# Kernel optimization log

Hardware: AMD Instinct MI355X
Metric: run time of the kernel (lower is better)

The kernel has to match this reference:

```python
import jax, jax.numpy as jnp
import numpy as np

KH, KW = 3, 3
KN = KH * KW  # kernel_n = 9


def _grid_offset(H, W):
    # Faithful to TF build(): stack(meshgrid(ij)).reshape(-1, 2) -- note this
    # interleaves i- and j- grids in an unusual layout; we replicate it exactly.
    init = jnp.stack(jnp.meshgrid(jnp.arange(KH), jnp.arange(KW), indexing='ij'))
    init = init.reshape(-1, 2).astype(jnp.float32)  # (KN, 2)
    ph, pw = (KH - 1) // 2, (KW - 1) // 2
    g = jnp.stack(
        jnp.meshgrid(jnp.arange(-ph, H - ph), jnp.arange(-pw, W - pw), indexing='ij'),
        axis=-1,
    ).astype(jnp.float32)  # (H, W, 2)
    return g[:, :, None, :] + init[None, None]  # (H, W, KN, 2)


def _bilinear_sample(x, coords):
    # x: (B, H, W, C); coords: (B, H, W, KN, 2) with (row, col) float coords.
    B = x.shape[0]
    y, xc = coords[..., 0], coords[..., 1]
    y0 = jnp.floor(y).astype(jnp.int32)
    y1 = jnp.ceil(y).astype(jnp.int32)   # ceil (not floor+1), faithful to TF code
    x0 = jnp.floor(xc).astype(jnp.int32)
    x1 = jnp.ceil(xc).astype(jnp.int32)
    bidx = jnp.arange(B)[:, None, None, None]

    def g(yy, xx):
        return x[bidx, yy, xx]  # (B, H, W, KN, C)

    v_lt = g(y0, x0)
    v_rb = g(y1, x1)
    v_lb = g(y0, x1)  # (lt_row, rb_col) per TF coords_lb
    v_rt = g(y1, x0)  # (rb_row, lt_col) per TF coords_rt
    fy = (y - y0.astype(y.dtype))[..., None]
    fx = (xc - x0.astype(xc.dtype))[..., None]
    v_t = v_lt + (v_rt - v_lt) * fy
    v_b = v_lb + (v_rb - v_lb) * fy
    return v_t + (v_b - v_t) * fx  # (B, H, W, KN, C)


def setup_inputs() -> dict:
    key = jax.random.key(0)
    k1, k2, k3 = jax.random.split(key, 3)
    B, H, W, C, F = 8, 64, 64, 128, 128
    x = jax.random.normal(k1, (B, H, W, C), dtype=jnp.float32)
    offset = jax.random.normal(k2, (B, H, W, 2 * KN), dtype=jnp.float32)
    Wk = jax.random.truncated_normal(k3, -2.0, 2.0, (KN, C, F), dtype=jnp.float32) * 0.02
    b = jnp.zeros((F,), dtype=jnp.float32)
    return {"x": x, "offset": offset, "W": Wk, "b": b}


def reference(x, offset, W, b):
    B, H, Wd, C = x.shape
    coords = _grid_offset(H, Wd)[None] + offset.reshape(B, H, Wd, KN, 2)
    coords = jnp.stack(
        [
            jnp.clip(coords[..., 0], 0.0, float(H - 1)),
            jnp.clip(coords[..., 1], 0.0, float(Wd - 1)),
        ],
        axis=-1,
    )
    deform = _bilinear_sample(x, coords)  # (B, H, W, KN, C)
    # conv3d with (1,1,KN,C,F) filter, VALID == contraction over (KN, C)
    out = jnp.einsum('bhwnc,ncf->bhwf', deform, W) + b
    return out
```

## Files before the change

### kernel.cpp

```cpp
#include <hip/hip_runtime.h>
#include <stdint.h>

#define KN 9
#define HH 64
#define WW 64
#define CC 128
#define FF 128
#define TM 64
#define NT 512
#define LDK 136

typedef __bf16 bf16x8 __attribute__((ext_vector_type(8)));
typedef float f32x4 __attribute__((ext_vector_type(4)));
typedef unsigned short us8 __attribute__((ext_vector_type(8)));
typedef unsigned short us4 __attribute__((ext_vector_type(4)));

__constant__ float c_init_i[KN] = {0.f,0.f,1.f,2.f,2.f,1.f,0.f,2.f,1.f};
__constant__ float c_init_j[KN] = {0.f,1.f,1.f,2.f,0.f,2.f,1.f,0.f,2.f};

static __device__ inline unsigned short f2bf(float f) {
    union { float f; unsigned u; } v; v.f = f;
    unsigned r = v.u + 0x7fffu + ((v.u >> 16) & 1u);
    return (unsigned short)(r >> 16);
}

__global__ void wt_kernel(const float* __restrict__ Wk, unsigned short* __restrict__ Wt) {
    __shared__ unsigned short t[32][33];
    const int tid = threadIdx.x;
    const int n  = blockIdx.x >> 4;
    const int tf = blockIdx.x & 3;
    const int tc = (blockIdx.x >> 2) & 3;
    const int g  = tid >> 5;
    const int l  = tid & 31;
#pragma unroll
    for (int r = 0; r < 4; ++r) {
        int cl = g * 4 + r;
        t[cl][l] = f2bf(Wk[(n << 14) + ((tc * 32 + cl) << 7) + (tf * 32 + l)]);
    }
    __syncthreads();
#pragma unroll
    for (int r = 0; r < 4; ++r) {
        int fl = g * 4 + r;
        Wt[(n << 14) + ((tf * 32 + fl) << 7) + (tc * 32 + l)] = t[l][fl];
    }
}

__launch_bounds__(NT, 4)
__global__ void deform_kernel(const float* __restrict__ xin,
                              const float* __restrict__ off,
                              const unsigned short* __restrict__ Wt,
                              const float* __restrict__ bias,
                              float* __restrict__ out) {
    __shared__ unsigned short As[TM][LDK];
    __shared__ unsigned short Bt[FF][LDK];
    __shared__ float cY[TM][KN];
    __shared__ float cX[TM][KN];

    const int tid = threadIdx.x;
    const int bb   = blockIdx.x & 7;
    const int hh   = blockIdx.x >> 3;
    const int pix0 = (bb << 12) + (hh << 6);

    for (int t = tid; t < TM * KN; t += NT) {
        int p = t & (TM - 1);
        int n = t >> 6;
        const float* op = off + (size_t)(pix0 + p) * (2 * KN) + 2 * n;
        float y = (float)(hh - 1) + c_init_i[n] + op[0];
        float x = (float)(p - 1) + c_init_j[n] + op[1];
        cY[p][n] = fminf(fmaxf(y, 0.f), 63.f);
        cX[p][n] = fminf(fmaxf(x, 0.f), 63.f);
    }
    __syncthreads();

    const int wave = tid >> 6;
    const int lane = tid & 63;
    const int quad = lane >> 4;
    const int col  = lane & 15;
    const int mtile = (wave & 1) * 32;
    const int ntile = (wave >> 1) * 32;

    f32x4 acc[2][2];
#pragma unroll
    for (int a = 0; a < 2; ++a)
#pragma unroll
        for (int b = 0; b < 2; ++b) acc[a][b] = (f32x4){0.f, 0.f, 0.f, 0.f};

    const float* bbase = xin + ((size_t)bb << 19);

    auto issue_gather = [&](int n, int k, float4* pf) {
        int i  = tid + k * NT;
        int p  = i >> 5;
        int cg = (i & 31) * 4;
        float y = cY[p][n], x = cX[p][n];
        int y0 = (int)floorf(y), x0 = (int)floorf(x);
        int y1 = (int)ceilf(y),  x1 = (int)ceilf(x);
        pf[0] = *(const float4*)(bbase + ((((y0 << 6) + x0) << 7) + cg));
        pf[1] = *(const float4*)(bbase + ((((y1 << 6) + x0) << 7) + cg));
        pf[2] = *(const float4*)(bbase + ((((y0 << 6) + x1) << 7) + cg));
        pf[3] = *(const float4*)(bbase + ((((y1 << 6) + x1) << 7) + cg));
    };
    auto consume = [&](int n, int k, const float4* pf) {
        int i  = tid + k * NT;
        int p  = i >> 5;
        int cg = (i & 31) * 4;
        float y = cY[p][n], x = cX[p][n];
        float fy = y - floorf(y), fx = x - floorf(x);
        float r0, r1, r2, r3;
        { float vt = pf[0].x + (pf[1].x - pf[0].x) * fy; float vb = pf[2].x + (pf[3].x - pf[2].x) * fy; r0 = vt + (vb - vt) * fx; }
        { float vt = pf[0].y + (pf[1].y - pf[0].y) * fy; float vb = pf[2].y + (pf[3].y - pf[2].y) * fy; r1 = vt + (vb - vt) * fx; }
        { float vt = pf[0].z + (pf[1].z - pf[0].z) * fy; float vb = pf[2].z + (pf[3].z - pf[2].z) * fy; r2 = vt + (vb - vt) * fx; }
        { float vt = pf[0].w + (pf[1].w - pf[0].w) * fy; float vb = pf[2].w + (pf[3].w - pf[2].w) * fy; r3 = vt + (vb - vt) * fx; }
        us4 pk;
        pk.x = f2bf(r0); pk.y = f2bf(r1); pk.z = f2bf(r2); pk.w = f2bf(r3);
        *(us4*)&As[p][cg] = pk;
    };

    float4 pf0[4], pf1[4];
    us8 bpf[4];
    issue_gather(0, 0, pf0);
    issue_gather(0, 1, pf1);
#pragma unroll
    for (int k = 0; k < 4; ++k) {
        int i2 = tid + k * NT;
        bpf[k] = *(const us8*)(Wt + (i2 >> 4) * CC + (i2 & 15) * 8);
    }

    for (int n = 0; n < KN; ++n) {
        float4 pf2[4], pf3[4];
        issue_gather(n, 2, pf2);
        issue_gather(n, 3, pf3);
#pragma unroll
        for (int k = 0; k < 4; ++k) {
            int i2 = tid + k * NT;
            *(us8*)&Bt[i2 >> 4][(i2 & 15) * 8] = bpf[k];
        }
        consume(n, 0, pf0);
        consume(n, 1, pf1);
        consume(n, 2, pf2);
        consume(n, 3, pf3);
        __syncthreads();

        if (n + 1 < KN) {
            issue_gather(n + 1, 0, pf0);
            issue_gather(n + 1, 1, pf1);
            const unsigned short* Wn = Wt + (n + 1) * (CC * FF);
#pragma unroll
            for (int k = 0; k < 4; ++k) {
                int i2 = tid + k * NT;
                bpf[k] = *(const us8*)(Wn + (i2 >> 4) * CC + (i2 & 15) * 8);
            }
        }

#pragma unroll
        for (int ks = 0; ks < 4; ++ks) {
            bf16x8 a0 = __builtin_bit_cast(bf16x8, *(const us8*)(&As[mtile + col][ks * 32 + quad * 8]));
            bf16x8 a1 = __builtin_bit_cast(bf16x8, *(const us8*)(&As[mtile + 16 + col][ks * 32 + quad * 8]));
            bf16x8 b0 = __builtin_bit_cast(bf16x8, *(const us8*)(&Bt[ntile + col][ks * 32 + quad * 8]));
            bf16x8 b1 = __builtin_bit_cast(bf16x8, *(const us8*)(&Bt[ntile + 16 + col][ks * 32 + quad * 8]));
            acc[0][0] = __builtin_amdgcn_mfma_f32_16x16x32_bf16(a0, b0, acc[0][0], 0, 0, 0);
            acc[0][1] = __builtin_amdgcn_mfma_f32_16x16x32_bf16(a0, b1, acc[0][1], 0, 0, 0);
            acc[1][0] = __builtin_amdgcn_mfma_f32_16x16x32_bf16(a1, b0, acc[1][0], 0, 0, 0);
            acc[1][1] = __builtin_amdgcn_mfma_f32_16x16x32_bf16(a1, b1, acc[1][1], 0, 0, 0);
        }
        __syncthreads();
    }

#pragma unroll
    for (int b = 0; b < 2; ++b) {
        int f = ntile + b * 16 + col;
        float bv = bias[f];
#pragma unroll
        for (int a = 0; a < 2; ++a) {
#pragma unroll
            for (int r = 0; r < 4; ++r) {
                int pr = pix0 + mtile + a * 16 + quad * 4 + r;
                out[(size_t)pr * FF + f] = acc[a][b][r] + bv;
            }
        }
    }
}

extern "C" void kernel_launch(void* const* d_in, const int* in_sizes, int n_in,
                              void* d_out, int out_size, void* d_ws, size_t ws_size,
                              hipStream_t stream) {
    const float* x    = (const float*)d_in[0];
    const float* off  = (const float*)d_in[1];
    const float* Wk   = (const float*)d_in[2];
    const float* bias = (const float*)d_in[3];
    float* out = (float*)d_out;
    unsigned short* Wt = (unsigned short*)d_ws;

    wt_kernel<<<KN * 16, 256, 0, stream>>>(Wk, Wt);
    deform_kernel<<<(8 * HH * WW) / TM, NT, 0, stream>>>(x, off, Wt, bias, out);
}
```

Measured before the change: 104.9 us.

## Halve pixel tile, double-buffer A in LDS, load B fragments directly into registers

Measured after the change: 134.3 us. 1.28x slower.

```diff
diff --git a/kernel.cpp b/kernel.cpp
--- a/kernel.cpp
+++ b/kernel.cpp
@@ -6,12 +6,13 @@
 #define WW 64
 #define CC 128
 #define FF 128
-#define TM 64
-#define NT 512
+#define TM 32
+#define NT 256
 #define LDK 136
 
 typedef __bf16 bf16x8 __attribute__((ext_vector_type(8)));
 typedef float f32x4 __attribute__((ext_vector_type(4)));
+typedef float f32x2 __attribute__((ext_vector_type(2)));
 typedef unsigned short us8 __attribute__((ext_vector_type(8)));
 typedef unsigned short us4 __attribute__((ext_vector_type(4)));
 
@@ -51,24 +52,34 @@
                               const unsigned short* __restrict__ Wt,
                               const float* __restrict__ bias,
                               float* __restrict__ out) {
-    __shared__ unsigned short As[TM][LDK];
-    __shared__ unsigned short Bt[FF][LDK];
-    __shared__ float cY[TM][KN];
-    __shared__ float cX[TM][KN];
+    __shared__ unsigned short As[2][TM][LDK];
+    __shared__ int   sO[4][KN][TM];
+    __shared__ float sF[2][KN][TM];
 
     const int tid = threadIdx.x;
     const int bb   = blockIdx.x & 7;
-    const int hh   = blockIdx.x >> 3;
-    const int pix0 = (bb << 12) + (hh << 6);
+    const int idx  = blockIdx.x >> 3;
+    const int hh   = idx >> 1;
+    const int half = idx & 1;
+    const int pix0 = (bb << 12) + (hh << 6) + (half << 5);
 
     for (int t = tid; t < TM * KN; t += NT) {
         int p = t & (TM - 1);
-        int n = t >> 6;
+        int n = t >> 5;
         const float* op = off + (size_t)(pix0 + p) * (2 * KN) + 2 * n;
         float y = (float)(hh - 1) + c_init_i[n] + op[0];
-        float x = (float)(p - 1) + c_init_j[n] + op[1];
-        cY[p][n] = fminf(fmaxf(y, 0.f), 63.f);
-        cX[p][n] = fminf(fmaxf(x, 0.f), 63.f);
+        float x = (float)(half * 32 + p - 1) + c_init_j[n] + op[1];
+        y = fminf(fmaxf(y, 0.f), 63.f);
+        x = fminf(fmaxf(x, 0.f), 63.f);
+        float fy0 = floorf(y), fx0 = floorf(x);
+        int y0 = (int)fy0, x0 = (int)fx0;
+        int y1 = (int)ceilf(y), x1 = (int)ceilf(x);
+        sO[0][n][p] = ((y0 << 6) + x0) << 7;
+        sO[1][n][p] = ((y1 << 6) + x0) << 7;
+        sO[2][n][p] = ((y0 << 6) + x1) << 7;
+        sO[3][n][p] = ((y1 << 6) + x1) << 7;
+        sF[0][n][p] = y - fy0;
+        sF[1][n][p] = x - fx0;
     }
     __syncthreads();
 
@@ -76,8 +87,7 @@
     const int lane = tid & 63;
     const int quad = lane >> 4;
     const int col  = lane & 15;
-    const int mtile = (wave & 1) * 32;
-    const int ntile = (wave >> 1) * 32;
+    const int ntb  = wave * 32;
 
     f32x4 acc[2][2];
 #pragma unroll
@@ -87,93 +97,91 @@
 
     const float* bbase = xin + ((size_t)bb << 19);
 
-    auto issue_gather = [&](int n, int k, float4* pf) {
+    auto issueA = [&](int n, int k, float4* pf) {
         int i  = tid + k * NT;
         int p  = i >> 5;
         int cg = (i & 31) * 4;
-        float y = cY[p][n], x = cX[p][n];
-        int y0 = (int)floorf(y), x0 = (int)floorf(x);
-        int y1 = (int)ceilf(y),  x1 = (int)ceilf(x);
-        pf[0] = *(const float4*)(bbase + ((((y0 << 6) + x0) << 7) + cg));
-        pf[1] = *(const float4*)(bbase + ((((y1 << 6) + x0) << 7) + cg));
-        pf[2] = *(const float4*)(bbase + ((((y0 << 6) + x1) << 7) + cg));
-        pf[3] = *(const float4*)(bbase + ((((y1 << 6) + x1) << 7) + cg));
+        const float* bp = bbase + cg;
+        pf[0] = *(const float4*)(bp + sO[0][n][p]);
+        pf[1] = *(const float4*)(bp + sO[1][n][p]);
+        pf[2] = *(const float4*)(bp + sO[2][n][p]);
+        pf[3] = *(const float4*)(bp + sO[3][n][p]);
     };
-    auto consume = [&](int n, int k, const float4* pf) {
+    auto consumeA = [&](int n, int k, const float4* pf, int cur) {
         int i  = tid + k * NT;
         int p  = i >> 5;
         int cg = (i & 31) * 4;
-        float y = cY[p][n], x = cX[p][n];
-        float fy = y - floorf(y), fx = x - floorf(x);
-        float r0, r1, r2, r3;
-        { float vt = pf[0].x + (pf[1].x - pf[0].x) * fy; float vb = pf[2].x + (pf[3].x - pf[2].x) * fy; r0 = vt + (vb - vt) * fx; }
-        { float vt = pf[0].y + (pf[1].y - pf[0].y) * fy; float vb = pf[2].y + (pf[3].y - pf[2].y) * fy; r1 = vt + (vb - vt) * fx; }
-        { float vt = pf[0].z + (pf[1].z - pf[0].z) * fy; float vb = pf[2].z + (pf[3].z - pf[2].z) * fy; r2 = vt + (vb - vt) * fx; }
-        { float vt = pf[0].w + (pf[1].w - pf[0].w) * fy; float vb = pf[2].w + (pf[3].w - pf[2].w) * fy; r3 = vt + (vb - vt) * fx; }
+        float fy = sF[0][n][p], fx = sF[1][n][p];
+        f32x2 fy2 = {fy, fy}, fx2 = {fx, fx};
+        f32x2 lt0 = {pf[0].x, pf[0].y}, lt1 = {pf[0].z, pf[0].w};
+        f32x2 rt0 = {pf[1].x, pf[1].y}, rt1 = {pf[1].z, pf[1].w};
+        f32x2 lb0 = {pf[2].x, pf[2].y}, lb1 = {pf[2].z, pf[2].w};
+        f32x2 rb0 = {pf[3].x, pf[3].y}, rb1 = {pf[3].z, pf[3].w};
+        f32x2 vt0 = lt0 + (rt0 - lt0) * fy2;
+        f32x2 vt1 = lt1 + (rt1 - lt1) * fy2;
+        f32x2 vb0 = lb0 + (rb0 - lb0) * fy2;
+        f32x2 vb1 = lb1 + (rb1 - lb1) * fy2;
+        f32x2 r0 = vt0 + (vb0 - vt0) * fx2;
+        f32x2 r1 = vt1 + (vb1 - vt1) * fx2;
         us4 pk;
-        pk.x = f2bf(r0); pk.y = f2bf(r1); pk.z = f2bf(r2); pk.w = f2bf(r3);
-        *(us4*)&As[p][cg] = pk;
+        pk.x = f2bf(r0.x); pk.y = f2bf(r0.y); pk.z = f2bf(r1.x); pk.w = f2bf(r1.y);
+        *(us4*)&As[cur][p][cg] = pk;
     };
-
-    float4 pf0[4], pf1[4];
-    us8 bpf[4];
-    issue_gather(0, 0, pf0);
-    issue_gather(0, 1, pf1);
-#pragma unroll
-    for (int k = 0; k < 4; ++k) {
-        int i2 = tid + k * NT;
-        bpf[k] = *(const us8*)(Wt + (i2 >> 4) * CC + (i2 & 15) * 8);
-    }
+    auto loadB = [&](int n, us8* bq) {
+        const unsigned short* Wn = Wt + (n << 14);
+#pragma unroll
+        for (int sub = 0; sub < 2; ++sub)
+#pragma unroll
+            for (int ks = 0; ks < 4; ++ks)
+                bq[sub * 4 + ks] = *(const us8*)(Wn + (ntb + sub * 16 + col) * CC + ks * 32 + quad * 8);
+    };
+
+    float4 pA0[4], pA1[4];
+    us8 bcur[8], bnxt[8];
+    issueA(0, 0, pA0);
+    issueA(0, 1, pA1);
+    loadB(0, bcur);
 
     for (int n = 0; n < KN; ++n) {
-        float4 pf2[4], pf3[4];
-        issue_gather(n, 2, pf2);
-        issue_gather(n, 3, pf3);
-#pragma unroll
-        for (int k = 0; k < 4; ++k) {
-            int i2 = tid + k * NT;
-            *(us8*)&Bt[i2 >> 4][(i2 & 15) * 8] = bpf[k];
+        const int cur = n & 1;
+        float4 pA2[4], pA3[4];
+        issueA(n, 2, pA2);
+        issueA(n, 3, pA3);
+        consumeA(n, 0, pA0, cur);
+        consumeA(n, 1, pA1, cur);
+        consumeA(n, 2, pA2, cur);
+        consumeA(n, 3, pA3, cur);
+        if (n + 1 < KN) {
+            issueA(n + 1, 0, pA0);
+            issueA(n + 1, 1, pA1);
+            loadB(n + 1, bnxt);
         }
-        consume(n, 0, pf0);
-        consume(n, 1, pf1);
-        consume(n, 2, pf2);
-        consume(n, 3, pf3);
         __syncthreads();
 
-        if (n + 1 < KN) {
-            issue_gather(n + 1, 0, pf0);
-            issue_gather(n + 1, 1, pf1);
-            const unsigned short* Wn = Wt + (n + 1) * (CC * FF);
-#pragma unroll
-            for (int k = 0; k < 4; ++k) {
-                int i2 = tid + k * NT;
-                bpf[k] = *(const us8*)(Wn + (i2 >> 4) * CC + (i2 & 15) * 8);
-            }
-        }
-
 #pragma unroll
         for (int ks = 0; ks < 4; ++ks) {
-            bf16x8 a0 = __builtin_bit_cast(bf16x8, *(const us8*)(&As[mtile + col][ks * 32 + quad * 8]));
-            bf16x8 a1 = __builtin_bit_cast(bf16x8, *(const us8*)(&As[mtile + 16 + col][ks * 32 + quad * 8]));
-            bf16x8 b0 = __builtin_bit_cast(bf16x8, *(const us8*)(&Bt[ntile + col][ks * 32 + quad * 8]));
-            bf16x8 b1 = __builtin_bit_cast(bf16x8, *(const us8*)(&Bt[ntile + 16 + col][ks * 32 + quad * 8]));
+            bf16x8 a0 = __builtin_bit_cast(bf16x8, *(const us8*)(&As[cur][col][ks * 32 + quad * 8]));
+            bf16x8 a1 = __builtin_bit_cast(bf16x8, *(const us8*)(&As[cur][16 + col][ks * 32 + quad * 8]));
+            bf16x8 b0 = __builtin_bit_cast(bf16x8, bcur[ks]);
+            bf16x8 b1 = __builtin_bit_cast(bf16x8, bcur[4 + ks]);
             acc[0][0] = __builtin_amdgcn_mfma_f32_16x16x32_bf16(a0, b0, acc[0][0], 0, 0, 0);
             acc[0][1] = __builtin_amdgcn_mfma_f32_16x16x32_bf16(a0, b1, acc[0][1], 0, 0, 0);
             acc[1][0] = __builtin_amdgcn_mfma_f32_16x16x32_bf16(a1, b0, acc[1][0], 0, 0, 0);
             acc[1][1] = __builtin_amdgcn_mfma_f32_16x16x32_bf16(a1, b1, acc[1][1], 0, 0, 0);
         }
-        __syncthreads();
+#pragma unroll
+        for (int q = 0; q < 8; ++q) bcur[q] = bnxt[q];
     }
 
 #pragma unroll
     for (int b = 0; b < 2; ++b) {
-        int f = ntile + b * 16 + col;
+        int f = ntb + b * 16 + col;
         float bv = bias[f];
 #pragma unroll
         for (int a = 0; a < 2; ++a) {
 #pragma unroll
             for (int r = 0; r < 4; ++r) {
-                int pr = pix0 + mtile + a * 16 + quad * 4 + r;
+                int pr = pix0 + a * 16 + quad * 4 + r;
                 out[(size_t)pr * FF + f] = acc[a][b][r] + bv;
             }
         }
```

## Double-buffer A tile, load weights directly to registers, drop second barrier

Applied to the files above, without the earlier changes.

Result: slower. 128.5 us (+22.4%).

```diff
diff --git a/kernel.cpp b/kernel.cpp
--- a/kernel.cpp
+++ b/kernel.cpp
@@ -51,8 +51,7 @@
                               const unsigned short* __restrict__ Wt,
                               const float* __restrict__ bias,
                               float* __restrict__ out) {
-    __shared__ unsigned short As[TM][LDK];
-    __shared__ unsigned short Bt[FF][LDK];
+    __shared__ unsigned short As[2][TM][LDK];
     __shared__ float cY[TM][KN];
     __shared__ float cX[TM][KN];
 
@@ -87,7 +86,7 @@
 
     const float* bbase = xin + ((size_t)bb << 19);
 
-    auto issue_gather = [&](int n, int k, float4* pf) {
+    auto issueA = [&](int n, int k, float4* pf) {
         int i  = tid + k * NT;
         int p  = i >> 5;
         int cg = (i & 31) * 4;
@@ -99,7 +98,7 @@
         pf[2] = *(const float4*)(bbase + ((((y0 << 6) + x1) << 7) + cg));
         pf[3] = *(const float4*)(bbase + ((((y1 << 6) + x1) << 7) + cg));
     };
-    auto consume = [&](int n, int k, const float4* pf) {
+    auto consumeA = [&](int n, int k, const float4* pf, int cur) {
         int i  = tid + k * NT;
         int p  = i >> 5;
         int cg = (i & 31) * 4;
@@ -112,57 +111,42 @@
         { float vt = pf[0].w + (pf[1].w - pf[0].w) * fy; float vb = pf[2].w + (pf[3].w - pf[2].w) * fy; r3 = vt + (vb - vt) * fx; }
         us4 pk;
         pk.x = f2bf(r0); pk.y = f2bf(r1); pk.z = f2bf(r2); pk.w = f2bf(r3);
-        *(us4*)&As[p][cg] = pk;
+        *(us4*)&As[cur][p][cg] = pk;
     };
 
-    float4 pf0[4], pf1[4];
-    us8 bpf[4];
-    issue_gather(0, 0, pf0);
-    issue_gather(0, 1, pf1);
+    for (int n = 0; n < KN; ++n) {
+        const int cur = n & 1;
+        float4 pf0[4], pf1[4], pf2[4], pf3[4];
+        issueA(n, 0, pf0);
+        issueA(n, 1, pf1);
+        consumeA(n, 0, pf0, cur);
+        issueA(n, 2, pf2);
+        consumeA(n, 1, pf1, cur);
+        issueA(n, 3, pf3);
+        consumeA(n, 2, pf2, cur);
+        consumeA(n, 3, pf3, cur);
+
+        us8 bq[8];
+        const unsigned short* Wn = Wt + (n << 14);
 #pragma unroll
-    for (int k = 0; k < 4; ++k) {
-        int i2 = tid + k * NT;
-        bpf[k] = *(const us8*)(Wt + (i2 >> 4) * CC + (i2 & 15) * 8);
-    }
+        for (int sub = 0; sub < 2; ++sub)
+#pragma unroll
+            for (int ks = 0; ks < 4; ++ks)
+                bq[sub * 4 + ks] = *(const us8*)(Wn + (ntile + sub * 16 + col) * CC + ks * 32 + quad * 8);
 
-    for (int n = 0; n < KN; ++n) {
-        float4 pf2[4], pf3[4];
-        issue_gather(n, 2, pf2);
-        issue_gather(n, 3, pf3);
-#pragma unroll
-        for (int k = 0; k < 4; ++k) {
-            int i2 = tid + k * NT;
-            *(us8*)&Bt[i2 >> 4][(i2 & 15) * 8] = bpf[k];
-        }
-        consume(n, 0, pf0);
-        consume(n, 1, pf1);
-        consume(n, 2, pf2);
-        consume(n, 3, pf3);
         __syncthreads();
-
-        if (n + 1 < KN) {
-            issue_gather(n + 1, 0, pf0);
-            issue_gather(n + 1, 1, pf1);
-            const unsigned short* Wn = Wt + (n + 1) * (CC * FF);
-#pragma unroll
-            for (int k = 0; k < 4; ++k) {
-                int i2 = tid + k * NT;
-                bpf[k] = *(const us8*)(Wn + (i2 >> 4) * CC + (i2 & 15) * 8);
-            }
-        }
 
 #pragma unroll
         for (int ks = 0; ks < 4; ++ks) {
-            bf16x8 a0 = __builtin_bit_cast(bf16x8, *(const us8*)(&As[mtile + col][ks * 32 + quad * 8]));
-            bf16x8 a1 = __builtin_bit_cast(bf16x8, *(const us8*)(&As[mtile + 16 + col][ks * 32 + quad * 8]));
-            bf16x8 b0 = __builtin_bit_cast(bf16x8, *(const us8*)(&Bt[ntile + col][ks * 32 + quad * 8]));
-            bf16x8 b1 = __builtin_bit_cast(bf16x8, *(const us8*)(&Bt[ntile + 16 + col][ks * 32 + quad * 8]));
+            bf16x8 a0 = __builtin_bit_cast(bf16x8, *(const us8*)(&As[cur][mtile + col][ks * 32 + quad * 8]));
+            bf16x8 a1 = __builtin_bit_cast(bf16x8, *(const us8*)(&As[cur][mtile + 16 + col][ks * 32 + quad * 8]));
+            bf16x8 b0 = __builtin_bit_cast(bf16x8, bq[ks]);
+            bf16x8 b1 = __builtin_bit_cast(bf16x8, bq[4 + ks]);
             acc[0][0] = __builtin_amdgcn_mfma_f32_16x16x32_bf16(a0, b0, acc[0][0], 0, 0, 0);
             acc[0][1] = __builtin_amdgcn_mfma_f32_16x16x32_bf16(a0, b1, acc[0][1], 0, 0, 0);
             acc[1][0] = __builtin_amdgcn_mfma_f32_16x16x32_bf16(a1, b0, acc[1][0], 0, 0, 0);
             acc[1][1] = __builtin_amdgcn_mfma_f32_16x16x32_bf16(a1, b1, acc[1][1], 0, 0, 0);
         }
-        __syncthreads();
     }
 
 #pragma unroll
```

## Pre-convert input to bf16 and gather bf16 corners, dropping software prefetch

Applied to the files above, without the earlier changes.

New measurement: 106.1 us. Within noise of the previous version (+1.1%).

```diff
diff --git a/kernel.cpp b/kernel.cpp
--- a/kernel.cpp
+++ b/kernel.cpp
@@ -23,6 +23,18 @@
     unsigned r = v.u + 0x7fffu + ((v.u >> 16) & 1u);
     return (unsigned short)(r >> 16);
 }
+static __device__ inline float bf2f(unsigned short h) {
+    union { unsigned u; float f; } v; v.u = ((unsigned)h) << 16;
+    return v.f;
+}
+
+__global__ void xq_kernel(const float* __restrict__ x, unsigned short* __restrict__ xq) {
+    int idx = blockIdx.x * 256 + threadIdx.x;
+    const float4 v = ((const float4*)x)[idx];
+    us4 o;
+    o.x = f2bf(v.x); o.y = f2bf(v.y); o.z = f2bf(v.z); o.w = f2bf(v.w);
+    ((us4*)xq)[idx] = o;
+}
 
 __global__ void wt_kernel(const float* __restrict__ Wk, unsigned short* __restrict__ Wt) {
     __shared__ unsigned short t[32][33];
@@ -46,7 +58,7 @@
 }
 
 __launch_bounds__(NT, 4)
-__global__ void deform_kernel(const float* __restrict__ xin,
+__global__ void deform_kernel(const unsigned short* __restrict__ xq,
                               const float* __restrict__ off,
                               const unsigned short* __restrict__ Wt,
                               const float* __restrict__ bias,
@@ -85,71 +97,51 @@
 #pragma unroll
         for (int b = 0; b < 2; ++b) acc[a][b] = (f32x4){0.f, 0.f, 0.f, 0.f};
 
-    const float* bbase = xin + ((size_t)bb << 19);
+    const unsigned short* bbase = xq + ((size_t)bb << 19);
 
-    auto issue_gather = [&](int n, int k, float4* pf) {
+    auto issueA = [&](int n, int k, us8* pc) {
         int i  = tid + k * NT;
-        int p  = i >> 5;
-        int cg = (i & 31) * 4;
+        int p  = i >> 4;
+        int cg = (i & 15) * 8;
         float y = cY[p][n], x = cX[p][n];
         int y0 = (int)floorf(y), x0 = (int)floorf(x);
         int y1 = (int)ceilf(y),  x1 = (int)ceilf(x);
-        pf[0] = *(const float4*)(bbase + ((((y0 << 6) + x0) << 7) + cg));
-        pf[1] = *(const float4*)(bbase + ((((y1 << 6) + x0) << 7) + cg));
-        pf[2] = *(const float4*)(bbase + ((((y0 << 6) + x1) << 7) + cg));
-        pf[3] = *(const float4*)(bbase + ((((y1 << 6) + x1) << 7) + cg));
+        pc[0] = *(const us8*)(bbase + ((((y0 << 6) + x0) << 7) + cg));
+        pc[1] = *(const us8*)(bbase + ((((y1 << 6) + x0) << 7) + cg));
+        pc[2] = *(const us8*)(bbase + ((((y0 << 6) + x1) << 7) + cg));
+        pc[3] = *(const us8*)(bbase + ((((y1 << 6) + x1) << 7) + cg));
     };
-    auto consume = [&](int n, int k, const float4* pf) {
+    auto consumeA = [&](int n, int k, const us8* pc) {
         int i  = tid + k * NT;
-        int p  = i >> 5;
-        int cg = (i & 31) * 4;
+        int p  = i >> 4;
+        int cg = (i & 15) * 8;
         float y = cY[p][n], x = cX[p][n];
         float fy = y - floorf(y), fx = x - floorf(x);
-        float r0, r1, r2, r3;
-        { float vt = pf[0].x + (pf[1].x - pf[0].x) * fy; float vb = pf[2].x + (pf[3].x - pf[2].x) * fy; r0 = vt + (vb - vt) * fx; }
-        { float vt = pf[0].y + (pf[1].y - pf[0].y) * fy; float vb = pf[2].y + (pf[3].y - pf[2].y) * fy; r1 = vt + (vb - vt) * fx; }
-        { float vt = pf[0].z + (pf[1].z - pf[0].z) * fy; float vb = pf[2].z + (pf[3].z - pf[2].z) * fy; r2 = vt + (vb - vt) * fx; }
-        { float vt = pf[0].w + (pf[1].w - pf[0].w) * fy; float vb = pf[2].w + (pf[3].w - pf[2].w) * fy; r3 = vt + (vb - vt) * fx; }
-        us4 pk;
-        pk.x = f2bf(r0); pk.y = f2bf(r1); pk.z = f2bf(r2); pk.w = f2bf(r3);
-        *(us4*)&As[p][cg] = pk;
+        us8 pk;
+#pragma unroll
+        for (int c = 0; c < 8; ++c) {
+            float vlt = bf2f(pc[0][c]), vrt = bf2f(pc[1][c]);
+            float vlb = bf2f(pc[2][c]), vrb = bf2f(pc[3][c]);
+            float vt = vlt + (vrt - vlt) * fy;
+            float vb = vlb + (vrb - vlb) * fy;
+            pk[c] = f2bf(vt + (vb - vt) * fx);
+        }
+        *(us8*)&As[p][cg] = pk;
     };
 
-    float4 pf0[4], pf1[4];
-    us8 bpf[4];
-    issue_gather(0, 0, pf0);
-    issue_gather(0, 1, pf1);
-#pragma unroll
-    for (int k = 0; k < 4; ++k) {
-        int i2 = tid + k * NT;
-        bpf[k] = *(const us8*)(Wt + (i2 >> 4) * CC + (i2 & 15) * 8);
-    }
-
     for (int n = 0; n < KN; ++n) {
-        float4 pf2[4], pf3[4];
-        issue_gather(n, 2, pf2);
-        issue_gather(n, 3, pf3);
+        const unsigned short* Wn = Wt + n * (CC * FF);
 #pragma unroll
         for (int k = 0; k < 4; ++k) {
             int i2 = tid + k * NT;
-            *(us8*)&Bt[i2 >> 4][(i2 & 15) * 8] = bpf[k];
+            *(us8*)&Bt[i2 >> 4][(i2 & 15) * 8] = *(const us8*)(Wn + (i2 >> 4) * CC + (i2 & 15) * 8);
         }
-        consume(n, 0, pf0);
-        consume(n, 1, pf1);
-        consume(n, 2, pf2);
-        consume(n, 3, pf3);
+        us8 u0[4], u1[4];
+        issueA(n, 0, u0);
+        issueA(n, 1, u1);
+        consumeA(n, 0, u0);
+        consumeA(n, 1, u1);
         __syncthreads();
-
-        if (n + 1 < KN) {
-            issue_gather(n + 1, 0, pf0);
-            issue_gather(n + 1, 1, pf1);
-            const unsigned short* Wn = Wt + (n + 1) * (CC * FF);
-#pragma unroll
-            for (int k = 0; k < 4; ++k) {
-                int i2 = tid + k * NT;
-                bpf[k] = *(const us8*)(Wn + (i2 >> 4) * CC + (i2 & 15) * 8);
-            }
-        }
 
 #pragma unroll
         for (int ks = 0; ks < 4; ++ks) {
@@ -189,7 +181,9 @@
     const float* bias = (const float*)d_in[3];
     float* out = (float*)d_out;
     unsigned short* Wt = (unsigned short*)d_ws;
+    unsigned short* xq = (unsigned short*)d_ws + (KN * CC * FF);
 
     wt_kernel<<<KN * 16, 256, 0, stream>>>(Wk, Wt);
-    deform_kernel<<<(8 * HH * WW) / TM, NT, 0, stream>>>(x, off, Wt, bias, out);
+    xq_kernel<<<(8 * HH * WW * CC) / 4 / 256, 256, 0, stream>>>(x, xq);
+    deform_kernel<<<(8 * HH * WW) / TM, NT, 0, stream>>>(xq, off, Wt, bias, out);
 }
```
